# Performance work log

Measured on AMD Instinct MI355X. Metric: run time of the kernel, lower is better.

Reference implementation:

```python
import math
import jax, jax.numpy as jnp
import numpy as np

B, DIM, H = 16, 1024, 16
HD = DIM // H                      # 64
P_ORIG = 1024                      # num_patches arg
NP = math.ceil(math.sqrt(P_ORIG)) ** 2 // 2   # 512 attended tokens
ALPHA, BETA, GAMMA = 1.9, 3.8, 15.2           # iRPE euc config, ratio=1.9
NUM_BUCKETS = 2 * int(BETA) + 1               # 7


def _rp_bucket(L):
    """Static euclidean-distance relative-position buckets (iRPE 'euc')."""
    E = int(math.ceil(math.sqrt(L)))
    flat = np.arange(E * E)
    pos = np.stack([flat // E, flat % E], axis=1)[:L].astype(np.float64)  # [L,2]
    diff = pos[:, None, :] - pos[None, :, :]
    dis = np.round(np.sqrt((diff ** 2).sum(-1)))
    far = np.round(ALPHA + np.log(np.maximum(dis, 1e-9) / ALPHA)
                   / math.log(GAMMA / ALPHA) * (BETA - ALPHA))
    idx = np.where(dis <= ALPHA, np.round(dis), np.minimum(far, BETA)).astype(np.int32)
    idx = idx - idx.min()
    return jnp.asarray(idx)  # [L,L] int32 in [0, int(BETA)]

RP_BUCKET = _rp_bucket(NP)


def setup_inputs() -> dict:
    key = jax.random.key(0)
    ks = jax.random.split(key, 7)
    s = 0.02
    return {
        "x": jax.random.normal(ks[0], (B, P_ORIG, DIM), dtype=jnp.float32),
        "wq": jax.random.normal(ks[1], (DIM, DIM), dtype=jnp.float32) * s,
        "wk": jax.random.normal(ks[2], (DIM, DIM), dtype=jnp.float32) * s,
        "wv": jax.random.normal(ks[3], (DIM, DIM), dtype=jnp.float32) * s,
        "rpe_w": jax.random.normal(ks[4], (HD, NUM_BUCKETS), dtype=jnp.float32) * s,
        "proj_w": jax.random.normal(ks[5], (DIM, DIM), dtype=jnp.float32) * s,
        "proj_b": jax.random.normal(ks[6], (DIM,), dtype=jnp.float32) * s,
    }


def reference(x, wq, wk, wv, rpe_w, proj_w, proj_b):
    # F.pad on token axis with pad = NP - N (negative => crop)
    pad = NP - x.shape[1]
    if pad >= 0:
        x = jnp.pad(x, ((0, 0), (0, pad), (0, 0)))
    else:
        x = x[:, :NP, :]
    b = x.shape[0]
    scale = HD ** (-0.5)

    def heads(t):  # [b,NP,DIM] -> [b,H,NP,HD]
        return t.reshape(b, NP, H, HD).transpose(0, 2, 1, 3)

    q = heads(x @ wq.T)
    k = heads(x @ wk.T)
    v = heads(x @ wv.T)

    attn = jnp.einsum('bhid,bhjd->bhij', q, k) * scale
    # contextual RPE on keys (transposed): bias[b,h,i,j] = q[b,h,i,:] . W[:, bucket[i,j]]
    lt = jnp.einsum('bhid,dn->bhin', q, rpe_w)                 # [b,H,NP,NB]
    bias = jnp.take_along_axis(lt, RP_BUCKET[None, None, :, :], axis=3)  # [b,H,NP,NP]
    attn = jax.nn.softmax(attn + bias, axis=-1)

    out = jnp.einsum('bhij,bhjd->bhid', attn, v)
    out = out.transpose(0, 2, 1, 3).reshape(b, NP, DIM)
    out = out @ proj_w.T + proj_b
    return out[:, :P_ORIG, :]
```

## Files before the change

kernel.cpp:

```cpp
#include <hip/hip_runtime.h>

typedef __attribute__((ext_vector_type(8))) __bf16 bf16x8;
typedef __attribute__((ext_vector_type(4))) float f32x4;

#define DEVI static __device__ __forceinline__

DEVI unsigned short f2bf(float f) {
  unsigned int u = __float_as_uint(f);
  u += 0x7fffu + ((u >> 16) & 1u);
  return (unsigned short)(u >> 16);
}
DEVI float bf2f(unsigned short s) {
  return __uint_as_float(((unsigned int)s) << 16);
}

union Frag {
  bf16x8 v;
  __bf16 hf[8];
  unsigned short h[8];
  unsigned int w[4];
};

typedef __attribute__((address_space(1))) const void gv_t;
typedef __attribute__((address_space(3))) void sv_t;
#define GLOAD_LDS16(gp, lp) __builtin_amdgcn_global_load_lds((gv_t*)(gp), (sv_t*)(lp), 16, 0, 0)

#define QSCALE 0.18033688011112042f

__global__ __launch_bounds__(256) void k_prep(
    const float* __restrict__ x, const float* __restrict__ wq,
    const float* __restrict__ wk, const float* __restrict__ wv,
    const float* __restrict__ pw,
    unsigned short* __restrict__ xb, unsigned short* __restrict__ wb,
    unsigned char* __restrict__ bkt)
{
  int t = blockIdx.x * 256 + threadIdx.x;
  if (t >= 1572864) {
    int q = t - 1572864;
    int i = q >> 9, j = q & 511;
    int ir = i / 23, ic = i - ir * 23;
    int jr = j / 23, jc = j - jr * 23;
    int dy = ir - jr, dx = ic - jc;
    double dis = rint(sqrt((double)(dy * dy + dx * dx)));
    int v;
    if (dis <= 1.9) {
      v = (int)rint(dis);
    } else {
      double far = rint(1.9 + log(dis / 1.9) * (1.9 / log(8.0)));
      v = (int)fmin(far, 3.8);
    }
    bkt[q] = (unsigned char)v;
    return;
  }
  const float* src;
  unsigned short* dst;
  if (t < 1048576) {
    long e0 = (long)t << 3;
    int m = (int)(e0 >> 10), cc = (int)(e0 & 1023);
    int b = m >> 9, i = m & 511;
    src = x + (((long)(b << 10) + i) << 10) + cc;
    dst = xb + ((long)m << 10) + cc;
  } else {
    long e0 = (long)(t - 1048576) << 3;
    int mat = (int)(e0 >> 20);
    long off = e0 & 1048575;
    const float* s = (mat == 0) ? wq : (mat == 1) ? wk : (mat == 2) ? wv : pw;
    src = s + off;
    dst = wb + e0;
  }
  float4 a = *(const float4*)src;
  float4 b4 = *(const float4*)(src + 4);
  uint4 o;
  o.x = f2bf(a.x)  | ((unsigned)f2bf(a.y)  << 16);
  o.y = f2bf(a.z)  | ((unsigned)f2bf(a.w)  << 16);
  o.z = f2bf(b4.x) | ((unsigned)f2bf(b4.y) << 16);
  o.w = f2bf(b4.z) | ((unsigned)f2bf(b4.w) << 16);
  *(uint4*)dst = o;
}

template<int MODE>
__global__ __launch_bounds__(512) void k_gemm(
    const unsigned short* __restrict__ A,
    const unsigned short* __restrict__ Bw,
    unsigned short* __restrict__ qh, unsigned short* __restrict__ kh,
    unsigned short* __restrict__ vt,
    float* __restrict__ out, const float* __restrict__ bias)
{
  __shared__ unsigned short sL[3 * 12288];

  const int NTN = (MODE == 0) ? 24 : 8;
  const int nwg = (MODE == 0) ? 768 : 256;
  const int cpx = nwg / 8;
  const int bid = blockIdx.x;
  const int swz = (bid & 7) * cpx + (bid >> 3);
  const int tileN = swz % NTN, tileM = swz / NTN;

  const int tid = threadIdx.x;
  const int w = tid >> 6, lane = tid & 63;
  const int g = lane >> 4, c = lane & 15;
  const int wm = w >> 1, wn = w & 1;

  const int sk = (g * 8) ^ ((c & 8) ? 16 : 0);
  int offA[4], offB[4];
#pragma unroll
  for (int i = 0; i < 4; ++i) {
    offA[i] = (wm * 4 + i) * 512 + c * 32 + sk;
    offB[i] = 8192 + (wn * 4 + i) * 512 + c * 32 + sk;
  }

  const int colb = ((lane & 3) * 8) ^ ((lane >= 32) ? 16 : 0);
  const unsigned short* gA0 = A  + ((long)(tileM * 256 + w * 32 + (lane >> 2))) * 1024 + colb;
  const unsigned short* gA1 = gA0 + 16 * 1024;
  const unsigned short* gB0 = Bw + ((long)(tileN * 128 + w * 16 + (lane >> 2))) * 1024 + colb;

#define STAGE(ktile, buf) do {                                             \
    const long ko_ = (long)(ktile) * 32;                                   \
    char* base_ = (char*)sL + (buf) * 24576;                               \
    GLOAD_LDS16(gA0 + ko_, base_ + (w * 2) * 1024 + lane * 16);            \
    GLOAD_LDS16(gA1 + ko_, base_ + (w * 2 + 1) * 1024 + lane * 16);        \
    GLOAD_LDS16(gB0 + ko_, base_ + 16384 + w * 1024 + lane * 16);          \
  } while (0)

  f32x4 acc[4][4] = {};

  STAGE(0, 0);
  STAGE(1, 1);

  int rb = 0, wbuf = 2;
  for (int t = 0; t < 32; ++t) {
    asm volatile("s_waitcnt vmcnt(3)" ::: "memory");
    __builtin_amdgcn_s_barrier();
    int kt = t + 2; if (kt > 31) kt = 31;
    STAGE(kt, wbuf);

    const unsigned short* lb = sL + rb * 12288;
    bf16x8 af[4], bf[4];
#pragma unroll
    for (int i = 0; i < 4; ++i) af[i] = *(const bf16x8*)(lb + offA[i]);
#pragma unroll
    for (int i = 0; i < 4; ++i) bf[i] = *(const bf16x8*)(lb + offB[i]);

    __builtin_amdgcn_s_setprio(1);
#pragma unroll
    for (int mi = 0; mi < 4; ++mi)
#pragma unroll
      for (int ni = 0; ni < 4; ++ni)
        acc[mi][ni] = __builtin_amdgcn_mfma_f32_16x16x32_bf16(af[mi], bf[ni], acc[mi][ni], 0, 0, 0);
    __builtin_amdgcn_s_setprio(0);
    asm volatile("s_waitcnt lgkmcnt(0)" ::: "memory");

    rb = (rb == 2) ? 0 : rb + 1;
    wbuf = (wbuf == 2) ? 0 : wbuf + 1;
  }
  asm volatile("s_waitcnt vmcnt(0)" ::: "memory");
#undef STAGE

  const int m0 = tileM * 256 + wm * 64;
  const int n0 = tileN * 128 + wn * 64;

  if (MODE == 0) {
#pragma unroll
    for (int mi = 0; mi < 4; ++mi) {
      int mrow = m0 + mi * 16 + g * 4;
      int b = mrow >> 9, i = mrow & 511;
#pragma unroll
      for (int ni = 0; ni < 4; ++ni) {
        int n = n0 + ni * 16 + c;
        int mat = n >> 10;
        int cc = n & 1023;
        int h = cc >> 6, d = cc & 63;
        long bh = (long)(b * 16 + h);
        if (mat == 2) {
          unsigned int w0 = f2bf(acc[mi][ni][0]) | ((unsigned)f2bf(acc[mi][ni][1]) << 16);
          unsigned int w1 = f2bf(acc[mi][ni][2]) | ((unsigned)f2bf(acc[mi][ni][3]) << 16);
          *(uint2*)(vt + (bh * 64 + d) * 512 + i) = make_uint2(w0, w1);
        } else {
          float sc = (mat == 0) ? QSCALE : 1.0f;
          unsigned short* dst = (mat == 0 ? qh : kh) + (bh * 512 + i) * 64 + d;
#pragma unroll
          for (int r = 0; r < 4; ++r)
            dst[(long)r * 64] = f2bf(acc[mi][ni][r] * sc);
        }
      }
    }
  } else {
#pragma unroll
    for (int mi = 0; mi < 4; ++mi) {
      int mrow = m0 + mi * 16 + g * 4;
#pragma unroll
      for (int ni = 0; ni < 4; ++ni) {
        int n = n0 + ni * 16 + c;
        float bv = bias[n];
#pragma unroll
        for (int r = 0; r < 4; ++r)
          out[(long)(mrow + r) * 1024 + n] = acc[mi][ni][r] + bv;
      }
    }
  }
}

__global__ __launch_bounds__(512) void k_attn(
    const unsigned short* __restrict__ qh, const unsigned short* __restrict__ kh,
    const unsigned short* __restrict__ vt, const float* __restrict__ rpe,
    const unsigned char* __restrict__ bkt, unsigned short* __restrict__ ao)
{
  __shared__ float lt_lds[512 * 9];
  const int head = blockIdx.x;
  const int b = head >> 4, h = head & 15;
  const int w = threadIdx.x >> 6, lane = threadIdx.x & 63;
  const int g = lane >> 4, c = lane & 15;
  const int qbase = w * 64;
  const unsigned short* Q = qh + (long)head * 512 * 64;
  const unsigned short* K = kh + (long)head * 512 * 64;
  const unsigned short* V = vt + (long)head * 64 * 512;

  Frag qu[4][2];
#pragma unroll
  for (int it = 0; it < 4; ++it)
#pragma unroll
    for (int kk = 0; kk < 2; ++kk)
      qu[it][kk].v = *(const bf16x8*)(Q + (qbase + it * 16 + c) * 64 + kk * 32 + g * 8);

  float lt[4][7] = {};
#pragma unroll
  for (int kk = 0; kk < 2; ++kk)
#pragma unroll
    for (int tt = 0; tt < 8; ++tt) {
      int d = kk * 32 + g * 8 + tt;
      const float* rr = rpe + d * 7;
      float r0 = rr[0], r1 = rr[1], r2 = rr[2], r3 = rr[3], r4 = rr[4], r5 = rr[5], r6 = rr[6];
#pragma unroll
      for (int it = 0; it < 4; ++it) {
        float qv = bf2f(qu[it][kk].h[tt]);
        lt[it][0] += qv * r0; lt[it][1] += qv * r1; lt[it][2] += qv * r2;
        lt[it][3] += qv * r3; lt[it][4] += qv * r4; lt[it][5] += qv * r5;
        lt[it][6] += qv * r6;
      }
    }
#pragma unroll
  for (int it = 0; it < 4; ++it)
#pragma unroll
    for (int n = 0; n < 7; ++n) {
      float v = lt[it][n];
      v += __shfl_xor(v, 16);
      v += __shfl_xor(v, 32);
      if (g == 0) lt_lds[(qbase + it * 16 + c) * 9 + n] = v * 8.0f;
    }

  int rowb36[4];
  const unsigned char* bktp[4];
#pragma unroll
  for (int it = 0; it < 4; ++it) {
    int row = qbase + it * 16 + c;
    rowb36[it] = row * 36;
    bktp[it] = bkt + (long)row * 512 + g * 8;
  }

  f32x4 oacc[4][4] = {};
  float lp[4] = {0.f, 0.f, 0.f, 0.f};
  const int jperm = (c >> 2) * 8 + (c & 3);

  for (int jb = 0; jb < 512; jb += 32) {
    const int jp0 = jb + jperm;
    Frag kf[2][2];
#pragma unroll
    for (int jt = 0; jt < 2; ++jt)
#pragma unroll
      for (int kk = 0; kk < 2; ++kk)
        kf[jt][kk].v = *(const bf16x8*)(K + (jp0 + jt * 4) * 64 + kk * 32 + g * 8);

    uint2 bb[4];
#pragma unroll
    for (int it = 0; it < 4; ++it)
      bb[it] = *(const uint2*)(bktp[it] + jb);

    f32x4 s[2][4];
#pragma unroll
    for (int jt = 0; jt < 2; ++jt)
#pragma unroll
      for (int it = 0; it < 4; ++it) {
        f32x4 z = {0.f, 0.f, 0.f, 0.f};
        z = __builtin_amdgcn_mfma_f32_16x16x32_bf16(kf[jt][0].v, qu[it][0].v, z, 0, 0, 0);
        s[jt][it] = __builtin_amdgcn_mfma_f32_16x16x32_bf16(kf[jt][1].v, qu[it][1].v, z, 0, 0, 0);
      }

    Frag pfr[4];
#pragma unroll
    for (int it = 0; it < 4; ++it) {
      float ps = 0.f;
#pragma unroll
      for (int jt = 0; jt < 2; ++jt) {
        unsigned int bw = jt ? bb[it].y : bb[it].x;
#pragma unroll
        for (int r = 0; r < 4; ++r) {
          int bno = (bw >> (8 * r)) & 255;
          float bias = *(const float*)((const char*)lt_lds + rowb36[it] + (bno << 2));
          float sv = s[jt][it][r] + bias;
          float p;
          asm("v_exp_f32 %0, %1" : "=v"(p) : "v"(sv));
          ps += p;
          pfr[it].hf[jt * 4 + r] = (__bf16)p;
        }
      }
      lp[it] += ps;
    }

    bf16x8 vf[4];
#pragma unroll
    for (int dt = 0; dt < 4; ++dt)
      vf[dt] = *(const bf16x8*)(V + (dt * 16 + c) * 512 + jb + g * 8);

#pragma unroll
    for (int dt = 0; dt < 4; ++dt)
#pragma unroll
      for (int it = 0; it < 4; ++it)
        oacc[dt][it] = __builtin_amdgcn_mfma_f32_16x16x32_bf16(vf[dt], pfr[it].v, oacc[dt][it], 0, 0, 0);
  }

  float li[4];
#pragma unroll
  for (int it = 0; it < 4; ++it) {
    float v = lp[it];
    v += __shfl_xor(v, 16);
    v += __shfl_xor(v, 32);
    li[it] = 1.0f / v;
  }
#pragma unroll
  for (int dt = 0; dt < 4; ++dt)
#pragma unroll
    for (int it = 0; it < 4; ++it) {
      int irow = qbase + it * 16 + c;
      int d0 = dt * 16 + g * 4;
      unsigned int w0 = f2bf(oacc[dt][it][0] * li[it]) | ((unsigned)f2bf(oacc[dt][it][1] * li[it]) << 16);
      unsigned int w1 = f2bf(oacc[dt][it][2] * li[it]) | ((unsigned)f2bf(oacc[dt][it][3] * li[it]) << 16);
      *(uint2*)(ao + ((long)(b * 512 + irow)) * 1024 + h * 64 + d0) = make_uint2(w0, w1);
    }
}

extern "C" void kernel_launch(void* const* d_in, const int* in_sizes, int n_in,
                              void* d_out, int out_size, void* d_ws, size_t ws_size,
                              hipStream_t stream) {
  const float* x   = (const float*)d_in[0];
  const float* wq  = (const float*)d_in[1];
  const float* wk  = (const float*)d_in[2];
  const float* wv  = (const float*)d_in[3];
  const float* rpe = (const float*)d_in[4];
  const float* pw  = (const float*)d_in[5];
  const float* pb  = (const float*)d_in[6];
  float* out = (float*)d_out;

  char* ws = (char*)d_ws;
  unsigned short* xb  = (unsigned short*)(ws);
  unsigned short* wb  = (unsigned short*)(ws + 16777216);
  unsigned short* qhp = (unsigned short*)(ws + 25165824);
  unsigned short* khp = (unsigned short*)(ws + 41943040);
  unsigned short* vtp = (unsigned short*)(ws + 58720256);
  unsigned char*  bkt = (unsigned char*)(ws + 75497472);
  unsigned short* aop = xb;

  k_prep<<<dim3(7168), dim3(256), 0, stream>>>(x, wq, wk, wv, pw, xb, wb, bkt);
  k_gemm<0><<<dim3(768), dim3(512), 0, stream>>>(xb, wb, qhp, khp, vtp, nullptr, nullptr);
  k_attn<<<dim3(256), dim3(512), 0, stream>>>(qhp, khp, vtp, rpe, bkt, aop);
  k_gemm<1><<<dim3(256), dim3(512), 0, stream>>>(aop, wb + 3 * 1048576, nullptr, nullptr, nullptr, out, pb);
}
```

Baseline: 151.6 us.

## Use 256x256 tiles with double-buffered LDS pipeline for QKV GEMM

Replaces the templated QKV projection GEMM with a dedicated kernel using 256x256 output tiles (384 workgroups instead of 768), 8 warps each computing a 128x64 subtile. K-chunks of 64 are double-buffered in 128KB of LDS, with global-to-LDS loads interleaved between MFMA halves. The aim is more operand reuse per byte loaded and better overlap of memory traffic with compute. In exchange it uses far more LDS and accumulator registers, which caps occupancy at one workgroup per CU and leaves fewer workgroups to fill the GPU.

```diff
diff --git a/kernel.cpp b/kernel.cpp
--- a/kernel.cpp
+++ b/kernel.cpp
@@ -78,22 +78,129 @@
   *(uint4*)dst = o;
 }
 
-template<int MODE>
-__global__ __launch_bounds__(512) void k_gemm(
+__global__ __launch_bounds__(512) void k_gemm8(
     const unsigned short* __restrict__ A,
     const unsigned short* __restrict__ Bw,
     unsigned short* __restrict__ qh, unsigned short* __restrict__ kh,
-    unsigned short* __restrict__ vt,
+    unsigned short* __restrict__ vt)
+{
+  __shared__ unsigned short sL[65536];
+
+  const int bid = blockIdx.x;
+  const int swz = (bid & 7) * 48 + (bid >> 3);
+  const int tileN = swz % 12, tileM = swz / 12;
+
+  const int t = threadIdx.x;
+  const int w = t >> 6, lane = t & 63;
+  const int g = lane >> 4, c = lane & 15;
+  const int wm = w >> 2, wn = w & 3;
+
+  const char* lbase = (const char*)sL;
+  const int cb = c * 64 + ((g * 16) ^ ((c & 8) ? 32 : 0));
+  const int aoffbase = wm * 8 * 1024 + cb;
+  const int boffbase = 32768 + wn * 4 * 1024 + cb;
+
+  const int rowb = (t >> 6) * 16 + ((t >> 2) & 15);
+  const int colb = ((t & 3) * 8) ^ (((t >> 2) & 8) ? 16 : 0);
+  const unsigned short* sAp = A  + (long)(tileM * 256 + rowb) * 1024 + colb;
+  const unsigned short* sBp = Bw + (long)(tileN * 256 + rowb) * 1024 + colb;
+  char* ldst = (char*)sL + t * 16;
+
+  f32x4 acc[8][4] = {};
+
+#define STG2(s, kn, obuf) do {                                              \
+    GLOAD_LDS16(sAp + (kn) * 64 + ((s) & 1) * 131072 + ((s) >> 1) * 32,     \
+                ldst + (obuf) + (s) * 8192);                                \
+    GLOAD_LDS16(sBp + (kn) * 64 + ((s) & 1) * 131072 + ((s) >> 1) * 32,     \
+                ldst + (obuf) + 32768 + (s) * 8192);                        \
+  } while (0)
+
+#define HALF(bufb_, kk, s0, s1, kn_, ob_) do {                              \
+    asm volatile("s_waitcnt vmcnt(4)" ::: "memory");                        \
+    __builtin_amdgcn_s_barrier();                                           \
+    bf16x8 aa[4], bb[4];                                                    \
+    _Pragma("unroll")                                                       \
+    for (int q_ = 0; q_ < 4; ++q_) {                                        \
+      aa[q_] = *(const bf16x8*)(lbase + (bufb_) + (kk) * 16384 + aoffbase + q_ * 1024); \
+      bb[q_] = *(const bf16x8*)(lbase + (bufb_) + (kk) * 16384 + boffbase + q_ * 1024); \
+    }                                                                       \
+    STG2(s0, kn_, ob_);                                                     \
+    __builtin_amdgcn_s_setprio(1);                                          \
+    _Pragma("unroll")                                                       \
+    for (int mi_ = 0; mi_ < 4; ++mi_)                                       \
+      _Pragma("unroll")                                                     \
+      for (int ni_ = 0; ni_ < 4; ++ni_)                                     \
+        acc[mi_][ni_] = __builtin_amdgcn_mfma_f32_16x16x32_bf16(aa[mi_], bb[ni_], acc[mi_][ni_], 0, 0, 0); \
+    __builtin_amdgcn_s_setprio(0);                                          \
+    bf16x8 a2[4];                                                           \
+    _Pragma("unroll")                                                       \
+    for (int q_ = 0; q_ < 4; ++q_)                                          \
+      a2[q_] = *(const bf16x8*)(lbase + (bufb_) + (kk) * 16384 + aoffbase + (4 + q_) * 1024); \
+    STG2(s1, kn_, ob_);                                                     \
+    __builtin_amdgcn_s_setprio(1);                                          \
+    _Pragma("unroll")                                                       \
+    for (int mi_ = 0; mi_ < 4; ++mi_)                                       \
+      _Pragma("unroll")                                                     \
+      for (int ni_ = 0; ni_ < 4; ++ni_)                                     \
+        acc[4 + mi_][ni_] = __builtin_amdgcn_mfma_f32_16x16x32_bf16(a2[mi_], bb[ni_], acc[4 + mi_][ni_], 0, 0, 0); \
+    __builtin_amdgcn_s_setprio(0);                                          \
+  } while (0)
+
+#define KTILE(bufv, kc) do {                                                \
+    HALF(bufv, 0, 0, 1, (kc) + 1, (bufv) ^ 65536);                          \
+    HALF(bufv, 1, 2, 3, (kc) + 1, (bufv) ^ 65536);                          \
+  } while (0)
+
+  STG2(0, 0, 0); STG2(1, 0, 0); STG2(2, 0, 0); STG2(3, 0, 0);
+
+#pragma unroll 1
+  for (int kc = 0; kc < 16; kc += 2) {
+    KTILE(0, kc);
+    KTILE(65536, kc + 1);
+  }
+  asm volatile("s_waitcnt vmcnt(0)" ::: "memory");
+#undef KTILE
+#undef HALF
+#undef STG2
+
+  const int m0 = tileM * 256 + wm * 128;
+  const int n0 = tileN * 256 + wn * 64;
+#pragma unroll
+  for (int mi = 0; mi < 8; ++mi) {
+    int mrow = m0 + mi * 16 + g * 4;
+    int b = mrow >> 9, i = mrow & 511;
+#pragma unroll
+    for (int ni = 0; ni < 4; ++ni) {
+      int n = n0 + ni * 16 + c;
+      int mat = n >> 10;
+      int cc = n & 1023;
+      int h = cc >> 6, d = cc & 63;
+      long bh = (long)(b * 16 + h);
+      if (mat == 2) {
+        unsigned int w0 = f2bf(acc[mi][ni][0]) | ((unsigned)f2bf(acc[mi][ni][1]) << 16);
+        unsigned int w1 = f2bf(acc[mi][ni][2]) | ((unsigned)f2bf(acc[mi][ni][3]) << 16);
+        *(uint2*)(vt + (bh * 64 + d) * 512 + i) = make_uint2(w0, w1);
+      } else {
+        float sc = (mat == 0) ? QSCALE : 1.0f;
+        unsigned short* dst = (mat == 0 ? qh : kh) + (bh * 512 + i) * 64 + d;
+#pragma unroll
+        for (int r = 0; r < 4; ++r)
+          dst[(long)r * 64] = f2bf(acc[mi][ni][r] * sc);
+      }
+    }
+  }
+}
+
+__global__ __launch_bounds__(512) void k_gemm_proj(
+    const unsigned short* __restrict__ A,
+    const unsigned short* __restrict__ Bw,
     float* __restrict__ out, const float* __restrict__ bias)
 {
   __shared__ unsigned short sL[3 * 12288];
 
-  const int NTN = (MODE == 0) ? 24 : 8;
-  const int nwg = (MODE == 0) ? 768 : 256;
-  const int cpx = nwg / 8;
   const int bid = blockIdx.x;
-  const int swz = (bid & 7) * cpx + (bid >> 3);
-  const int tileN = swz % NTN, tileM = swz / NTN;
+  const int swz = (bid & 7) * 32 + (bid >> 3);
+  const int tileN = swz % 8, tileM = swz / 8;
 
   const int tid = threadIdx.x;
   const int w = tid >> 6, lane = tid & 63;
@@ -157,44 +264,16 @@
 
   const int m0 = tileM * 256 + wm * 64;
   const int n0 = tileN * 128 + wn * 64;
-
-  if (MODE == 0) {
-#pragma unroll
-    for (int mi = 0; mi < 4; ++mi) {
-      int mrow = m0 + mi * 16 + g * 4;
-      int b = mrow >> 9, i = mrow & 511;
-#pragma unroll
-      for (int ni = 0; ni < 4; ++ni) {
-        int n = n0 + ni * 16 + c;
-        int mat = n >> 10;
-        int cc = n & 1023;
-        int h = cc >> 6, d = cc & 63;
-        long bh = (long)(b * 16 + h);
-        if (mat == 2) {
-          unsigned int w0 = f2bf(acc[mi][ni][0]) | ((unsigned)f2bf(acc[mi][ni][1]) << 16);
-          unsigned int w1 = f2bf(acc[mi][ni][2]) | ((unsigned)f2bf(acc[mi][ni][3]) << 16);
-          *(uint2*)(vt + (bh * 64 + d) * 512 + i) = make_uint2(w0, w1);
-        } else {
-          float sc = (mat == 0) ? QSCALE : 1.0f;
-          unsigned short* dst = (mat == 0 ? qh : kh) + (bh * 512 + i) * 64 + d;
-#pragma unroll
-          for (int r = 0; r < 4; ++r)
-            dst[(long)r * 64] = f2bf(acc[mi][ni][r] * sc);
-        }
-      }
-    }
-  } else {
-#pragma unroll
-    for (int mi = 0; mi < 4; ++mi) {
-      int mrow = m0 + mi * 16 + g * 4;
-#pragma unroll
-      for (int ni = 0; ni < 4; ++ni) {
-        int n = n0 + ni * 16 + c;
-        float bv = bias[n];
-#pragma unroll
-        for (int r = 0; r < 4; ++r)
-          out[(long)(mrow + r) * 1024 + n] = acc[mi][ni][r] + bv;
-      }
+#pragma unroll
+  for (int mi = 0; mi < 4; ++mi) {
+    int mrow = m0 + mi * 16 + g * 4;
+#pragma unroll
+    for (int ni = 0; ni < 4; ++ni) {
+      int n = n0 + ni * 16 + c;
+      float bv = bias[n];
+#pragma unroll
+      for (int r = 0; r < 4; ++r)
+        out[(long)(mrow + r) * 1024 + n] = acc[mi][ni][r] + bv;
     }
   }
 }
@@ -359,7 +438,7 @@
   unsigned short* aop = xb;
 
   k_prep<<<dim3(7168), dim3(256), 0, stream>>>(x, wq, wk, wv, pw, xb, wb, bkt);
-  k_gemm<0><<<dim3(768), dim3(512), 0, stream>>>(xb, wb, qhp, khp, vtp, nullptr, nullptr);
+  k_gemm8<<<dim3(384), dim3(512), 0, stream>>>(xb, wb, qhp, khp, vtp);
   k_attn<<<dim3(256), dim3(512), 0, stream>>>(qhp, khp, vtp, rpe, bkt, aop);
-  k_gemm<1><<<dim3(256), dim3(512), 0, stream>>>(aop, wb + 3 * 1048576, nullptr, nullptr, nullptr, out, pb);
-}
+  k_gemm_proj<<<dim3(256), dim3(512), 0, stream>>>(aop, wb + 3 * 1048576, out, pb);
+}
```

New measurement: 153.8 us. Within noise of the previous version (+1.5%).

## Use a dedicated 256x192-tile double-buffered QKV GEMM kernel

Applied to the files above, without the earlier changes.

Splits the templated GEMM into a dedicated QKV projection kernel and a projection kernel. The QKV kernel uses 256x192 tiles (512 workgroups instead of 768), a 4x2 wave layout with 8x3 accumulators per wave, BK=64 double buffering and an XOR-swizzled LDS layout. Loads for the next tile are interleaved between MFMA groups. The goal is more reuse per byte loaded and fewer workgroups, at the cost of more registers and a larger LDS footprint, which lowers occupancy.

```diff
diff --git a/kernel.cpp b/kernel.cpp
--- a/kernel.cpp
+++ b/kernel.cpp
@@ -78,22 +78,170 @@
   *(uint4*)dst = o;
 }
 
-template<int MODE>
-__global__ __launch_bounds__(512) void k_gemm(
+__global__ __launch_bounds__(512) void k_gemm8(
     const unsigned short* __restrict__ A,
     const unsigned short* __restrict__ Bw,
     unsigned short* __restrict__ qh, unsigned short* __restrict__ kh,
-    unsigned short* __restrict__ vt,
+    unsigned short* __restrict__ vt)
+{
+  __shared__ unsigned short sL[2 * 28672];
+
+  const int bid = blockIdx.x;
+  const int swz = (bid & 7) * 64 + (bid >> 3);
+  const int tileN = swz & 15, tileM = swz >> 4;
+
+  const int t = threadIdx.x;
+  const int w = t >> 6, lane = t & 63;
+  const int g4 = lane >> 4, c = lane & 15;
+  const int wm = w >> 2, wn = w & 3;
+
+  const char* lbase = (const char*)sL;
+  const int acb = c * 64 + ((g4 * 16) ^ ((c & 8) ? 32 : 0));
+  const int aoffbase = wm * 8192 + acb;
+  int boff[3][2];
+#pragma unroll
+  for (int ni = 0; ni < 3; ++ni) {
+    int row = wn * 48 + ni * 16 + c;
+    int base = 32768 + (row >> 6) * 8192 + (row & 63) * 128;
+    int rx = row & 7;
+#pragma unroll
+    for (int kk = 0; kk < 2; ++kk)
+      boff[ni][kk] = base + (((kk * 4 + g4) ^ rx) << 4);
+  }
+
+  const int rowa = w * 16 + (lane >> 2);
+  const int cola = ((lane & 3) * 8) ^ (((lane >> 2) & 8) ? 16 : 0);
+  const unsigned short* sAp = A + (long)(tileM * 256 + rowa) * 1024 + cola;
+  char* ldsta = (char*)sL + t * 16;
+  const int rowbb = t >> 3;
+  const int colbb = ((t & 7) ^ ((t >> 3) & 7)) * 8;
+  const unsigned short* sBp = Bw + (long)(tileN * 192 + rowbb) * 1024 + colbb;
+  char* ldstb = (char*)sL + 32768 + t * 16;
+
+#define STGA(rh, kh, kn, ob) \
+  GLOAD_LDS16(sAp + (long)(kn) * 64 + (rh) * 131072 + (kh) * 32, \
+              ldsta + (ob) + (kh) * 16384 + (rh) * 8192)
+#define STGB(gg, kn, ob) \
+  GLOAD_LDS16(sBp + (long)(kn) * 64 + (gg) * 65536, \
+              ldstb + (ob) + (gg) * 8192)
+
+  f32x4 acc[8][3] = {};
+
+  STGA(0, 0, 0, 0); STGA(1, 0, 0, 0);
+  STGB(0, 0, 0); STGB(1, 0, 0); STGB(2, 0, 0);
+  STGA(0, 1, 0, 0); STGA(1, 1, 0, 0);
+
+#pragma unroll 1
+  for (int kt = 0; kt < 16; ++kt) {
+    const int cb = (kt & 1) ? 57344 : 0;
+    const int ob = cb ^ 57344;
+    const int kn = (kt < 15) ? kt + 1 : 15;
+
+    {
+      asm volatile("s_waitcnt vmcnt(2)" ::: "memory");
+      __builtin_amdgcn_s_barrier();
+      bf16x8 aa[4], bbf[3];
+#pragma unroll
+      for (int q = 0; q < 4; ++q)
+        aa[q] = *(const bf16x8*)(lbase + cb + aoffbase + q * 1024);
+#pragma unroll
+      for (int ni = 0; ni < 3; ++ni)
+        bbf[ni] = *(const bf16x8*)(lbase + cb + boff[ni][0]);
+      STGA(0, 0, kn, ob); STGA(1, 0, kn, ob); STGB(0, kn, ob);
+      __builtin_amdgcn_s_setprio(1);
+#pragma unroll
+      for (int mi = 0; mi < 4; ++mi)
+#pragma unroll
+        for (int ni = 0; ni < 3; ++ni)
+          acc[mi][ni] = __builtin_amdgcn_mfma_f32_16x16x32_bf16(aa[mi], bbf[ni], acc[mi][ni], 0, 0, 0);
+      __builtin_amdgcn_s_setprio(0);
+      bf16x8 a2[4];
+#pragma unroll
+      for (int q = 0; q < 4; ++q)
+        a2[q] = *(const bf16x8*)(lbase + cb + aoffbase + (4 + q) * 1024);
+      STGB(1, kn, ob); STGB(2, kn, ob);
+      __builtin_amdgcn_s_setprio(1);
+#pragma unroll
+      for (int mi = 0; mi < 4; ++mi)
+#pragma unroll
+        for (int ni = 0; ni < 3; ++ni)
+          acc[4 + mi][ni] = __builtin_amdgcn_mfma_f32_16x16x32_bf16(a2[mi], bbf[ni], acc[4 + mi][ni], 0, 0, 0);
+      __builtin_amdgcn_s_setprio(0);
+    }
+    {
+      asm volatile("s_waitcnt vmcnt(5)" ::: "memory");
+      __builtin_amdgcn_s_barrier();
+      bf16x8 aa[4], bbf[3];
+#pragma unroll
+      for (int q = 0; q < 4; ++q)
+        aa[q] = *(const bf16x8*)(lbase + cb + 16384 + aoffbase + q * 1024);
+#pragma unroll
+      for (int ni = 0; ni < 3; ++ni)
+        bbf[ni] = *(const bf16x8*)(lbase + cb + boff[ni][1]);
+      STGA(0, 1, kn, ob);
+      __builtin_amdgcn_s_setprio(1);
+#pragma unroll
+      for (int mi = 0; mi < 4; ++mi)
+#pragma unroll
+        for (int ni = 0; ni < 3; ++ni)
+          acc[mi][ni] = __builtin_amdgcn_mfma_f32_16x16x32_bf16(aa[mi], bbf[ni], acc[mi][ni], 0, 0, 0);
+      __builtin_amdgcn_s_setprio(0);
+      bf16x8 a2[4];
+#pragma unroll
+      for (int q = 0; q < 4; ++q)
+        a2[q] = *(const bf16x8*)(lbase + cb + 16384 + aoffbase + (4 + q) * 1024);
+      STGA(1, 1, kn, ob);
+      __builtin_amdgcn_s_setprio(1);
+#pragma unroll
+      for (int mi = 0; mi < 4; ++mi)
+#pragma unroll
+        for (int ni = 0; ni < 3; ++ni)
+          acc[4 + mi][ni] = __builtin_amdgcn_mfma_f32_16x16x32_bf16(a2[mi], bbf[ni], acc[4 + mi][ni], 0, 0, 0);
+      __builtin_amdgcn_s_setprio(0);
+    }
+  }
+  asm volatile("s_waitcnt vmcnt(0)" ::: "memory");
+#undef STGA
+#undef STGB
+
+  const int m0 = tileM * 256 + wm * 128;
+  const int n0 = tileN * 192 + wn * 48;
+#pragma unroll
+  for (int mi = 0; mi < 8; ++mi) {
+    int mrow = m0 + mi * 16 + g4 * 4;
+    int b = mrow >> 9, i = mrow & 511;
+#pragma unroll
+    for (int ni = 0; ni < 3; ++ni) {
+      int n = n0 + ni * 16 + c;
+      int mat = n >> 10;
+      int cc = n & 1023;
+      int h = cc >> 6, d = cc & 63;
+      long bh = (long)(b * 16 + h);
+      if (mat == 2) {
+        unsigned int w0 = f2bf(acc[mi][ni][0]) | ((unsigned)f2bf(acc[mi][ni][1]) << 16);
+        unsigned int w1 = f2bf(acc[mi][ni][2]) | ((unsigned)f2bf(acc[mi][ni][3]) << 16);
+        *(uint2*)(vt + (bh * 64 + d) * 512 + i) = make_uint2(w0, w1);
+      } else {
+        float sc = (mat == 0) ? QSCALE : 1.0f;
+        unsigned short* dst = (mat == 0 ? qh : kh) + (bh * 512 + i) * 64 + d;
+#pragma unroll
+        for (int r = 0; r < 4; ++r)
+          dst[(long)r * 64] = f2bf(acc[mi][ni][r] * sc);
+      }
+    }
+  }
+}
+
+__global__ __launch_bounds__(512) void k_gemm_proj(
+    const unsigned short* __restrict__ A,
+    const unsigned short* __restrict__ Bw,
     float* __restrict__ out, const float* __restrict__ bias)
 {
   __shared__ unsigned short sL[3 * 12288];
 
-  const int NTN = (MODE == 0) ? 24 : 8;
-  const int nwg = (MODE == 0) ? 768 : 256;
-  const int cpx = nwg / 8;
   const int bid = blockIdx.x;
-  const int swz = (bid & 7) * cpx + (bid >> 3);
-  const int tileN = swz % NTN, tileM = swz / NTN;
+  const int swz = (bid & 7) * 32 + (bid >> 3);
+  const int tileN = swz % 8, tileM = swz / 8;
 
   const int tid = threadIdx.x;
   const int w = tid >> 6, lane = tid & 63;
@@ -157,44 +305,16 @@
 
   const int m0 = tileM * 256 + wm * 64;
   const int n0 = tileN * 128 + wn * 64;
-
-  if (MODE == 0) {
-#pragma unroll
-    for (int mi = 0; mi < 4; ++mi) {
-      int mrow = m0 + mi * 16 + g * 4;
-      int b = mrow >> 9, i = mrow & 511;
-#pragma unroll
-      for (int ni = 0; ni < 4; ++ni) {
-        int n = n0 + ni * 16 + c;
-        int mat = n >> 10;
-        int cc = n & 1023;
-        int h = cc >> 6, d = cc & 63;
-        long bh = (long)(b * 16 + h);
-        if (mat == 2) {
-          unsigned int w0 = f2bf(acc[mi][ni][0]) | ((unsigned)f2bf(acc[mi][ni][1]) << 16);
-          unsigned int w1 = f2bf(acc[mi][ni][2]) | ((unsigned)f2bf(acc[mi][ni][3]) << 16);
-          *(uint2*)(vt + (bh * 64 + d) * 512 + i) = make_uint2(w0, w1);
-        } else {
-          float sc = (mat == 0) ? QSCALE : 1.0f;
-          unsigned short* dst = (mat == 0 ? qh : kh) + (bh * 512 + i) * 64 + d;
-#pragma unroll
-          for (int r = 0; r < 4; ++r)
-            dst[(long)r * 64] = f2bf(acc[mi][ni][r] * sc);
-        }
-      }
-    }
-  } else {
-#pragma unroll
-    for (int mi = 0; mi < 4; ++mi) {
-      int mrow = m0 + mi * 16 + g * 4;
-#pragma unroll
-      for (int ni = 0; ni < 4; ++ni) {
-        int n = n0 + ni * 16 + c;
-        float bv = bias[n];
-#pragma unroll
-        for (int r = 0; r < 4; ++r)
-          out[(long)(mrow + r) * 1024 + n] = acc[mi][ni][r] + bv;
-      }
+#pragma unroll
+  for (int mi = 0; mi < 4; ++mi) {
+    int mrow = m0 + mi * 16 + g * 4;
+#pragma unroll
+    for (int ni = 0; ni < 4; ++ni) {
+      int n = n0 + ni * 16 + c;
+      float bv = bias[n];
+#pragma unroll
+      for (int r = 0; r < 4; ++r)
+        out[(long)(mrow + r) * 1024 + n] = acc[mi][ni][r] + bv;
     }
   }
 }
@@ -359,7 +479,7 @@
   unsigned short* aop = xb;
 
   k_prep<<<dim3(7168), dim3(256), 0, stream>>>(x, wq, wk, wv, pw, xb, wb, bkt);
-  k_gemm<0><<<dim3(768), dim3(512), 0, stream>>>(xb, wb, qhp, khp, vtp, nullptr, nullptr);
+  k_gemm8<<<dim3(512), dim3(512), 0, stream>>>(xb, wb, qhp, khp, vtp);
   k_attn<<<dim3(256), dim3(512), 0, stream>>>(qhp, khp, vtp, rpe, bkt, aop);
-  k_gemm<1><<<dim3(256), dim3(512), 0, stream>>>(aop, wb + 3 * 1048576, nullptr, nullptr, nullptr, out, pb);
-}
+  k_gemm_proj<<<dim3(256), dim3(512), 0, stream>>>(aop, wb + 3 * 1048576, out, pb);
+}
```

New measurement: 154.5 us. About the same (+1.9%).
